# Kernel tuning notes

Measured on AMD Instinct MI355X. Metric: run time of the kernel, lower is better.

## Reference

```python
import jax, jax.numpy as jnp
import numpy as np

VOCAB = 32000
WDIM = 768      # bert-base hidden size, per self.w_dim
H = 512         # lstm_hidden
NUM_CAT = 5
START = 3       # l2ind['SOS']
END = 4         # l2ind['EOS']
T = 2048
NEG = -10000.0


def _lstm_dir(x, Wih, Whh, bih, bhh, reverse):
    # x: [T, WDIM]; torch LSTM gate order: i, f, g, o
    z_in = x @ Wih.T + bih + bhh  # [T, 4H] precompute input projection
    def step(carry, zt):
        h, c = carry
        z = zt + h @ Whh.T
        i, f, g, o = jnp.split(z, 4)
        c = jax.nn.sigmoid(f) * c + jax.nn.sigmoid(i) * jnp.tanh(g)
        h = jax.nn.sigmoid(o) * jnp.tanh(c)
        return (h, c), h
    init = (jnp.zeros((H,), x.dtype), jnp.zeros((H,), x.dtype))
    _, hs = jax.lax.scan(step, init, z_in, reverse=reverse)
    return hs  # [T, H], aligned with input order


def setup_inputs():
    key = jax.random.key(0)
    ks = jax.random.split(key, 13)
    s = 0.05
    sent = jax.random.randint(ks[0], (T,), 0, VOCAB)
    emb = jax.random.normal(ks[1], (VOCAB, WDIM), jnp.float32) * 0.02
    Wih_f = jax.random.normal(ks[2], (4 * H, WDIM), jnp.float32) * s
    Whh_f = jax.random.normal(ks[3], (4 * H, H), jnp.float32) * s
    bih_f = jax.random.normal(ks[4], (4 * H,), jnp.float32) * s
    bhh_f = jax.random.normal(ks[5], (4 * H,), jnp.float32) * s
    Wih_b = jax.random.normal(ks[6], (4 * H, WDIM), jnp.float32) * s
    Whh_b = jax.random.normal(ks[7], (4 * H, H), jnp.float32) * s
    bih_b = jax.random.normal(ks[8], (4 * H,), jnp.float32) * s
    bhh_b = jax.random.normal(ks[9], (4 * H,), jnp.float32) * s
    fc_w = jax.random.normal(ks[10], (NUM_CAT, 2 * H), jnp.float32) * s
    fc_b = jax.random.normal(ks[11], (NUM_CAT,), jnp.float32) * s
    transitions = jax.random.normal(ks[12], (NUM_CAT, NUM_CAT), jnp.float32)
    transitions = transitions.at[START, :].set(NEG).at[:, END].set(NEG)
    return {"sent": sent, "emb": emb,
            "Wih_f": Wih_f, "Whh_f": Whh_f, "bih_f": bih_f, "bhh_f": bhh_f,
            "Wih_b": Wih_b, "Whh_b": Whh_b, "bih_b": bih_b, "bhh_b": bhh_b,
            "fc_w": fc_w, "fc_b": fc_b, "transitions": transitions}


def reference(sent, emb, Wih_f, Whh_f, bih_f, bhh_f, Wih_b, Whh_b, bih_b, bhh_b, fc_w, fc_b, transitions):
    # _get_scores: embedding -> BiLSTM -> fc
    x = emb[sent]                                   # [T, WDIM]
    h_f = _lstm_dir(x, Wih_f, Whh_f, bih_f, bhh_f, reverse=False)
    h_b = _lstm_dir(x, Wih_b, Whh_b, bih_b, bhh_b, reverse=True)
    out = jnp.concatenate([h_f, h_b], axis=-1)      # [T, 2H]
    feats = out @ fc_w.T + fc_b                     # [T, NUM_CAT]

    # _viterbi_decode: transitions[i, j] = score of moving from tag j to tag i
    init = feats[0] + transitions[:, START]         # [NUM_CAT]
    def vstep(layer, feat_t):
        # scores[i, j] = feat_t[i] + transitions[i, j] + layer[j]
        scores = feat_t[:, None] + transitions + layer[None, :]
        return jnp.max(scores, axis=1), jnp.argmax(scores, axis=1)
    layer, parents = jax.lax.scan(vstep, init, feats[1:])  # parents: [T-1, NUM_CAT]

    final = layer + transitions[END]
    idx0 = jnp.argmax(final)
    path_score = jnp.max(final)

    # backtrack (parents[0] of the original loop is all-START and gets popped)
    def btrack(idx, p):
        nxt = p[idx]
        return nxt, nxt
    _, idxs = jax.lax.scan(btrack, idx0, parents, reverse=True)  # [T-1]
    path = jnp.concatenate([idxs, idx0[None]])      # [T]
    return path, path_score
```

## Files before the change

### kernel.cpp

```cpp
#include <hip/hip_runtime.h>

#define TT 2048
#define WD 768
#define HH 512
#define G4 2048
#define NC 5
#define SENT 0xFFFFFFFFu

typedef float f4 __attribute__((ext_vector_type(4)));
typedef unsigned int u4 __attribute__((ext_vector_type(4)));

__global__ __launch_bounds__(256) void zin_gemm(
    const int* __restrict__ sent, const float* __restrict__ emb,
    const float* __restrict__ Wih_f, const float* __restrict__ bih_f, const float* __restrict__ bhh_f,
    const float* __restrict__ Wih_b, const float* __restrict__ bih_b, const float* __restrict__ bhh_b,
    float* __restrict__ zin_f, float* __restrict__ zin_b)
{
    const int dirn = blockIdx.z;
    const float* Wih = dirn ? Wih_b : Wih_f;
    const float* bih = dirn ? bih_b : bih_f;
    const float* bhh = dirn ? bhh_b : bhh_f;
    float* zin = dirn ? zin_b : zin_f;

    __shared__ float As[16][128];
    __shared__ float Bs[16][128];

    const int tid = threadIdx.x;
    const int t0 = blockIdx.y * 128;
    const int g0 = blockIdx.x * 128;
    const int tm = tid >> 4, tn = tid & 15;

    float acc[8][8];
#pragma unroll
    for (int a = 0; a < 8; a++)
#pragma unroll
        for (int b = 0; b < 8; b++) acc[a][b] = 0.f;

    for (int kt = 0; kt < 48; ++kt) {
        const int k0 = kt * 16;
#pragma unroll
        for (int u = 0; u < 2; ++u) {
            const int s = tid * 2 + u;
            const int m = s >> 2, kq = s & 3;
            const int rowA = sent[t0 + m];
            float4 av = *(const float4*)(emb + (size_t)rowA * WD + k0 + kq * 4);
            As[kq * 4 + 0][m] = av.x; As[kq * 4 + 1][m] = av.y;
            As[kq * 4 + 2][m] = av.z; As[kq * 4 + 3][m] = av.w;
            float4 bv = *(const float4*)(Wih + (size_t)(g0 + m) * WD + k0 + kq * 4);
            Bs[kq * 4 + 0][m] = bv.x; Bs[kq * 4 + 1][m] = bv.y;
            Bs[kq * 4 + 2][m] = bv.z; Bs[kq * 4 + 3][m] = bv.w;
        }
        __syncthreads();
#pragma unroll
        for (int kk = 0; kk < 16; ++kk) {
            float4 a0 = *(const float4*)&As[kk][tm * 8];
            float4 a1 = *(const float4*)&As[kk][tm * 8 + 4];
            float4 b0 = *(const float4*)&Bs[kk][tn * 8];
            float4 b1 = *(const float4*)&Bs[kk][tn * 8 + 4];
            float av8[8] = {a0.x, a0.y, a0.z, a0.w, a1.x, a1.y, a1.z, a1.w};
            float bv8[8] = {b0.x, b0.y, b0.z, b0.w, b1.x, b1.y, b1.z, b1.w};
#pragma unroll
            for (int a = 0; a < 8; a++)
#pragma unroll
                for (int b = 0; b < 8; b++) acc[a][b] += av8[a] * bv8[b];
        }
        __syncthreads();
    }
    float bias[8];
#pragma unroll
    for (int b = 0; b < 8; b++) { int g = g0 + tn * 8 + b; bias[b] = bih[g] + bhh[g]; }
#pragma unroll
    for (int a = 0; a < 8; a++) {
        const int t = t0 + tm * 8 + a;
        float* op = zin + (size_t)t * G4 + g0 + tn * 8;
        float4 o0 = {acc[a][0] + bias[0], acc[a][1] + bias[1], acc[a][2] + bias[2], acc[a][3] + bias[3]};
        float4 o1 = {acc[a][4] + bias[4], acc[a][5] + bias[5], acc[a][6] + bias[6], acc[a][7] + bias[7]};
        *(float4*)op = o0; *(float4*)(op + 4) = o1;
    }
}

__global__ __launch_bounds__(256, 2) void lstm_rec(
    const float* __restrict__ zin_f, const float* __restrict__ zin_b,
    const float* __restrict__ Whh_f, const float* __restrict__ Whh_b,
    unsigned int* __restrict__ hw_f, unsigned int* __restrict__ hw_b,
    unsigned int* __restrict__ xcc)
{
    const int bid = blockIdx.x;
    const int lane8 = bid & 7;
    if (lane8 >= 2) return;
    const int d = lane8;
    const int k = bid >> 3;
    const float* zin = d ? zin_b : zin_f;
    const float* Whh = d ? Whh_b : Whh_f;
    unsigned int* hw = d ? hw_b : hw_f;

    const int tid = threadIdx.x;
    const int q = tid >> 6;
    const int r = tid & 63;
    const int gate = r >> 4, jj = r & 15;
    const int grow = gate * HH + k * 16 + jj;
    const f4* wrow = (const f4*)(Whh + (size_t)grow * HH + q * 128);

    f4 wa[20];
#pragma unroll
    for (int i = 0; i < 20; ++i) wa[i] = wrow[i];
#pragma unroll
    for (int i = 0; i < 20; ++i)
        asm volatile("" : "+a"(wa[i]));

    __shared__ f4 wl4[12 * 256];
    __shared__ float hs[HH];
    __shared__ float zb[256];
#pragma unroll
    for (int i = 0; i < 12; ++i) wl4[i * 256 + tid] = wrow[20 + i];

    unsigned int myxcc;
    asm volatile("s_getreg_b32 %0, hwreg(20, 0, 4)" : "=s"(myxcc));
    if (tid == 0)
        __hip_atomic_store(&xcc[d * 32 + k], myxcc,
                           __ATOMIC_RELAXED, __HIP_MEMORY_SCOPE_AGENT);
    __syncthreads();

    float c = 0.f;
    const int l = tid;
    const int g = l >> 4, j = l & 15;
    const int n16 = k * 16 + j;
    bool coU = false, coInit = false;

    for (int it = 0; it < TT; ++it) {
        const int t = d ? (TT - 1 - it) : it;

        float z = 0.f;
        if (tid < 64) z = zin[(size_t)t * G4 + g * HH + n16];

        if (it > 0 && tid < 64) {
            if (!coInit) {
                unsigned int px = __hip_atomic_load(&xcc[d * 32 + (l >> 1)],
                                                    __ATOMIC_RELAXED, __HIP_MEMORY_SCOPE_AGENT);
                unsigned long long mk = __ballot(px == myxcc);
                coU = (mk == 0xFFFFFFFFFFFFFFFFull);
                coInit = true;
            }
            const int tp = d ? (t + 1) : (t - 1);
            const unsigned int* pa = hw + (size_t)tp * HH + l * 8;
            u4 a0, a1;
            if (coU) {
                for (unsigned pi = 0;; ++pi) {
                    if ((pi & 3u) == 3u) {
                        asm volatile(
                            "global_load_dwordx4 %0, %2, off sc0 sc1\n\t"
                            "global_load_dwordx4 %1, %2, off offset:16 sc0 sc1\n\t"
                            "s_waitcnt vmcnt(0)"
                            : "=v"(a0), "=v"(a1) : "v"(pa) : "memory");
                    } else {
                        asm volatile(
                            "global_load_dwordx4 %0, %2, off sc0\n\t"
                            "global_load_dwordx4 %1, %2, off offset:16 sc0\n\t"
                            "s_waitcnt vmcnt(0)"
                            : "=v"(a0), "=v"(a1) : "v"(pa) : "memory");
                    }
                    if (a0.x != SENT && a0.y != SENT && a0.z != SENT && a0.w != SENT &&
                        a1.x != SENT && a1.y != SENT && a1.z != SENT && a1.w != SENT) break;
                }
            } else {
                for (;;) {
                    asm volatile(
                        "global_load_dwordx4 %0, %2, off sc0 sc1\n\t"
                        "global_load_dwordx4 %1, %2, off offset:16 sc0 sc1\n\t"
                        "s_waitcnt vmcnt(0)"
                        : "=v"(a0), "=v"(a1) : "v"(pa) : "memory");
                    if (a0.x != SENT && a0.y != SENT && a0.z != SENT && a0.w != SENT &&
                        a1.x != SENT && a1.y != SENT && a1.z != SENT && a1.w != SENT) break;
                }
            }
            u4* hd = (u4*)(hs + l * 8);
            hd[0] = a0; hd[1] = a1;
        }
        __syncthreads();

#pragma unroll
        for (int i = 0; i < 20; ++i) asm volatile("" : "+a"(wa[i]));

        float part = 0.f;
        if (it > 0) {
            const f4* hv = ((const f4*)hs) + (q << 5);
#pragma unroll
            for (int i = 0; i < 20; ++i) {
                f4 h4 = hv[i];
                part += wa[i].x * h4.x + wa[i].y * h4.y + wa[i].z * h4.z + wa[i].w * h4.w;
            }
#pragma unroll
            for (int i = 0; i < 12; ++i) {
                f4 h4 = hv[20 + i];
                f4 wv = wl4[i * 256 + tid];
                part += wv.x * h4.x + wv.y * h4.y + wv.z * h4.z + wv.w * h4.w;
            }
        }
        zb[tid] = part;
        __syncthreads();

        if (tid < 64) {
            float s = zb[l] + zb[64 + l] + zb[128 + l] + zb[192 + l];
            const float pre = z + s;
            float act;
            if (g == 2) act = tanhf(pre);
            else        act = 1.f / (1.f + expf(-pre));
            const float gi = __shfl(act, j);
            const float gf = __shfl(act, j + 16);
            const float gg = __shfl(act, j + 32);
            const float go = __shfl(act, j + 48);
            if (l < 16) {
                c = gf * c + gi * gg;
                const float hval = go * tanhf(c);
                __hip_atomic_store(&hw[(size_t)t * HH + k * 16 + l],
                                   __float_as_uint(hval),
                                   __ATOMIC_RELAXED, __HIP_MEMORY_SCOPE_AGENT);
            }
        }
    }
}

__global__ void feats_kernel(const float* __restrict__ h_f, const float* __restrict__ h_b,
                             const float* __restrict__ fc_w, const float* __restrict__ fc_b,
                             float* __restrict__ feats)
{
    const int t = blockIdx.x;
    const int l = threadIdx.x;
    float acc[NC] = {0.f, 0.f, 0.f, 0.f, 0.f};
    for (int m = 0; m < 16; ++m) {
        const int cg = l + m * 64;
        const float hv = (cg < HH) ? h_f[(size_t)t * HH + cg]
                                   : h_b[(size_t)t * HH + cg - HH];
#pragma unroll
        for (int i = 0; i < NC; i++) acc[i] += hv * fc_w[i * (2 * HH) + cg];
    }
#pragma unroll
    for (int i = 0; i < NC; i++) {
#pragma unroll
        for (int off = 32; off; off >>= 1) acc[i] += __shfl_xor(acc[i], off);
    }
    if (l == 0) {
#pragma unroll
        for (int i = 0; i < NC; i++) feats[(size_t)t * NC + i] = acc[i] + fc_b[i];
    }
}

__global__ void viterbi_kernel(const float* __restrict__ feats,
                               const float* __restrict__ trans,
                               float* __restrict__ out)
{
    __shared__ float fs[TT * NC];
    __shared__ int par[TT];
    __shared__ float pathv[TT];
    const int tid = threadIdx.x;
    for (int i = tid; i < TT * NC; i += 64) fs[i] = feats[i];
    float tr[25];
#pragma unroll
    for (int i = 0; i < 25; i++) tr[i] = trans[i];
    __syncthreads();

    float layer[NC];
#pragma unroll
    for (int i = 0; i < NC; i++) layer[i] = fs[i] + tr[i * 5 + 3];

    for (int s = 0; s < TT - 1; ++s) {
        const float* ft = &fs[(s + 1) * NC];
        float nl[NC]; int pk = 0;
#pragma unroll
        for (int i = 0; i < NC; i++) {
            float best = tr[i * 5 + 0] + layer[0]; int bj = 0;
#pragma unroll
            for (int jj = 1; jj < NC; jj++) {
                const float v = tr[i * 5 + jj] + layer[jj];
                if (v > best) { best = v; bj = jj; }
            }
            nl[i] = ft[i] + best;
            pk |= bj << (3 * i);
        }
#pragma unroll
        for (int i = 0; i < NC; i++) layer[i] = nl[i];
        if (tid == 0) par[s] = pk;
    }
    float best = layer[0] + tr[20]; int idx0 = 0;
#pragma unroll
    for (int jj = 1; jj < NC; jj++) {
        const float v = layer[jj] + tr[20 + jj];
        if (v > best) { best = v; idx0 = jj; }
    }
    __syncthreads();
    if (tid == 0) {
        pathv[TT - 1] = (float)idx0;
        int idx = idx0;
        for (int s = TT - 2; s >= 0; --s) {
            idx = (par[s] >> (3 * idx)) & 7;
            pathv[s] = (float)idx;
        }
        out[TT] = best;
    }
    __syncthreads();
    for (int i = tid; i < TT; i += 64) out[i] = pathv[i];
}

extern "C" void kernel_launch(void* const* d_in, const int* in_sizes, int n_in,
                              void* d_out, int out_size, void* d_ws, size_t ws_size,
                              hipStream_t stream) {
    const int*   sent   = (const int*)d_in[0];
    const float* emb    = (const float*)d_in[1];
    const float* Wih_f  = (const float*)d_in[2];
    const float* Whh_f  = (const float*)d_in[3];
    const float* bih_f  = (const float*)d_in[4];
    const float* bhh_f  = (const float*)d_in[5];
    const float* Wih_b  = (const float*)d_in[6];
    const float* Whh_b  = (const float*)d_in[7];
    const float* bih_b  = (const float*)d_in[8];
    const float* bhh_b  = (const float*)d_in[9];
    const float* fc_w   = (const float*)d_in[10];
    const float* fc_b   = (const float*)d_in[11];
    const float* trans  = (const float*)d_in[12];
    float* out = (float*)d_out;

    char* ws = (char*)d_ws;
    float* zin_f = (float*)ws;
    float* zin_b = (float*)(ws + (size_t)16777216);
    unsigned int* hw_f = (unsigned int*)(ws + (size_t)33554432);
    unsigned int* hw_b = (unsigned int*)(ws + (size_t)37748736);
    unsigned int* xcc  = (unsigned int*)(ws + (size_t)41943040);
    float* feats = (float*)(ws + (size_t)41947136);

    hipMemsetAsync(hw_f, 0xFF, (size_t)8388608 + 4096, stream);

    dim3 gg(G4 / 128, TT / 128, 2);
    zin_gemm<<<gg, 256, 0, stream>>>(sent, emb, Wih_f, bih_f, bhh_f,
                                     Wih_b, bih_b, bhh_b, zin_f, zin_b);

    lstm_rec<<<256, 256, 0, stream>>>(zin_f, zin_b, Whh_f, Whh_b, hw_f, hw_b, xcc);

    feats_kernel<<<TT, 64, 0, stream>>>((const float*)hw_f, (const float*)hw_b,
                                        fc_w, fc_b, feats);

    viterbi_kernel<<<1, 64, 0, stream>>>(feats, trans, out);
}
```

Measured before the change: 5.102 ms.

## Hold full Whh slice in AGPRs, split dot-product accumulators, tune spin polling

Each thread now keeps its whole 128-wide Whh row slice (32 float4) in accumulator registers instead of splitting it between registers and LDS, and the launch bound drops to one block per CU to allow the extra registers. The dot product uses four independent partial sums to shorten the dependency chain. The same-XCC spin loop forces the system-coherent load only every 16th iteration instead of every 4th, and the h store is written twice with different cache-scope bits. The aim is to shorten the per-timestep critical path of the serial recurrence, at the cost of more register pressure and possibly slower cross-CU visibility of h.

```diff
diff --git a/kernel.cpp b/kernel.cpp
--- a/kernel.cpp
+++ b/kernel.cpp
@@ -79,7 +79,7 @@
     }
 }
 
-__global__ __launch_bounds__(256, 2) void lstm_rec(
+__global__ __launch_bounds__(256, 1) void lstm_rec(
     const float* __restrict__ zin_f, const float* __restrict__ zin_b,
     const float* __restrict__ Whh_f, const float* __restrict__ Whh_b,
     unsigned int* __restrict__ hw_f, unsigned int* __restrict__ hw_b,
@@ -95,31 +95,28 @@
     unsigned int* hw = d ? hw_b : hw_f;
 
     const int tid = threadIdx.x;
-    const int q = tid >> 6;
-    const int r = tid & 63;
-    const int gate = r >> 4, jj = r & 15;
-    const int grow = gate * HH + k * 16 + jj;
-    const f4* wrow = (const f4*)(Whh + (size_t)grow * HH + q * 128);
-
-    f4 wa[20];
-#pragma unroll
-    for (int i = 0; i < 20; ++i) wa[i] = wrow[i];
-#pragma unroll
-    for (int i = 0; i < 20; ++i)
-        asm volatile("" : "+a"(wa[i]));
-
-    __shared__ f4 wl4[12 * 256];
-    __shared__ float hs[HH];
-    __shared__ float zb[256];
-#pragma unroll
-    for (int i = 0; i < 12; ++i) wl4[i * 256 + tid] = wrow[20 + i];
 
     unsigned int myxcc;
     asm volatile("s_getreg_b32 %0, hwreg(20, 0, 4)" : "=s"(myxcc));
     if (tid == 0)
         __hip_atomic_store(&xcc[d * 32 + k], myxcc,
                            __ATOMIC_RELAXED, __HIP_MEMORY_SCOPE_AGENT);
-    __syncthreads();
+
+    const int q = tid >> 6;
+    const int r = tid & 63;
+    const int gate = r >> 4, jj = r & 15;
+    const int grow = gate * HH + k * 16 + jj;
+
+    const f4* wp = (const f4*)(Whh + (size_t)grow * HH + q * 128);
+    f4 w[32];
+#pragma unroll
+    for (int i = 0; i < 32; ++i) w[i] = wp[i];
+#pragma unroll
+    for (int i = 0; i < 32; ++i)
+        asm volatile("" : "+a"(w[i]));
+
+    __shared__ float hs[HH];
+    __shared__ float zb[256];
 
     float c = 0.f;
     const int l = tid;
@@ -146,7 +143,7 @@
             u4 a0, a1;
             if (coU) {
                 for (unsigned pi = 0;; ++pi) {
-                    if ((pi & 3u) == 3u) {
+                    if ((pi & 15u) == 15u) {
                         asm volatile(
                             "global_load_dwordx4 %0, %2, off sc0 sc1\n\t"
                             "global_load_dwordx4 %1, %2, off offset:16 sc0 sc1\n\t"
@@ -179,22 +176,21 @@
         __syncthreads();
 
 #pragma unroll
-        for (int i = 0; i < 20; ++i) asm volatile("" : "+a"(wa[i]));
+        for (int i = 0; i < 32; ++i) asm volatile("" : "+a"(w[i]));
 
         float part = 0.f;
         if (it > 0) {
             const f4* hv = ((const f4*)hs) + (q << 5);
-#pragma unroll
-            for (int i = 0; i < 20; ++i) {
-                f4 h4 = hv[i];
-                part += wa[i].x * h4.x + wa[i].y * h4.y + wa[i].z * h4.z + wa[i].w * h4.w;
-            }
-#pragma unroll
-            for (int i = 0; i < 12; ++i) {
-                f4 h4 = hv[20 + i];
-                f4 wv = wl4[i * 256 + tid];
-                part += wv.x * h4.x + wv.y * h4.y + wv.z * h4.z + wv.w * h4.w;
-            }
+            float p0 = 0.f, p1 = 0.f, p2 = 0.f, p3 = 0.f;
+#pragma unroll
+            for (int i = 0; i < 8; ++i) {
+                f4 h0 = hv[i], h1 = hv[i + 8], h2 = hv[i + 16], h3 = hv[i + 24];
+                p0 += w[i].x      * h0.x + w[i].y      * h0.y + w[i].z      * h0.z + w[i].w      * h0.w;
+                p1 += w[i + 8].x  * h1.x + w[i + 8].y  * h1.y + w[i + 8].z  * h1.z + w[i + 8].w  * h1.w;
+                p2 += w[i + 16].x * h2.x + w[i + 16].y * h2.y + w[i + 16].z * h2.z + w[i + 16].w * h2.w;
+                p3 += w[i + 24].x * h3.x + w[i + 24].y * h3.y + w[i + 24].z * h3.z + w[i + 24].w * h3.w;
+            }
+            part = (p0 + p1) + (p2 + p3);
         }
         zb[tid] = part;
         __syncthreads();
@@ -212,9 +208,12 @@
             if (l < 16) {
                 c = gf * c + gi * gg;
                 const float hval = go * tanhf(c);
-                __hip_atomic_store(&hw[(size_t)t * HH + k * 16 + l],
-                                   __float_as_uint(hval),
-                                   __ATOMIC_RELAXED, __HIP_MEMORY_SCOPE_AGENT);
+                unsigned int* dst = &hw[(size_t)t * HH + k * 16 + l];
+                const unsigned int uval = __float_as_uint(hval);
+                asm volatile(
+                    "global_store_dword %0, %1, off sc0 sc1\n\t"
+                    "global_store_dword %0, %1, off sc0"
+                    :: "v"(dst), "v"(uval) : "memory");
             }
         }
     }
```

Result: slower. 8.317 ms (+63.0%).
